# Kernel optimization log

Hardware: AMD Instinct MI355X
Metric: run time of the kernel (lower is better)

## Reference

```python
import jax, jax.numpy as jnp
import numpy as np
from jax import lax

P = 192      # patches per frame
PS = 7       # patch size
GH, GW = 16, 16  # grid cells
DS = 4       # encoder downsize factor
CH = 128     # feature channels
KS, PAD = 7, 3  # harris avg-pool kernel / padding


def _encoder(x, w, b):
    # stand-in encoder: conv(1->CH, k=7, stride=DS, pad=3) + relu
    y = lax.conv_general_dilated(x, w, (DS, DS), [(PAD, PAD), (PAD, PAD)],
                                 dimension_numbers=('NCHW', 'OIHW', 'NCHW'))
    return jax.nn.relu(y + b[None, :, None, None])


def _harris(frame):
    b, n, c, h, w = frame.shape
    f = frame.reshape(b * n, c, h, w)
    dx = jnp.pad(f[..., 1:] - f[..., :-1], ((0, 0), (0, 0), (0, 0), (0, 1)), mode='reflect')
    dy = jnp.pad(f[..., 1:, :] - f[..., :-1, :], ((0, 0), (0, 0), (0, 1), (0, 0)), mode='reflect')
    def avg(x):
        s = lax.reduce_window(x, 0.0, lax.add, (1, 1, KS, KS), (1, 1, 1, 1),
                              [(0, 0), (0, 0), (PAD, PAD), (PAD, PAD)])
        return s / (KS * KS)  # count_include_pad=True like torch avg_pool2d
    Ixx, Iyy, Ixy = avg(dx * dx), avg(dy * dy), avg(dx * dy)
    return (Ixx * Iyy - Ixy * Ixy) / (Ixx + Iyy + 1e-8)


def _best_coords(g):
    bn, _, h, w = g.shape
    ph = -(-h // GH); pw = -(-w // GW)
    g = jnp.pad(g, ((0, 0), (0, 0), (0, ph * GH - h), (0, pw * GW - w)))
    g = g.reshape(bn, GH, ph, GW, pw).transpose(0, 1, 3, 2, 4).reshape(bn, GH, GW, ph * pw)
    idx = jnp.argmax(g, axis=-1)
    vals = jnp.max(g, axis=-1)
    yg = idx // pw + (ph * jnp.arange(GH))[None, :, None]
    xg = idx % pw + (pw * jnp.arange(GW))[None, None, :]
    _, top = lax.top_k(vals.reshape(bn, -1), P)
    yb = jnp.take_along_axis(yg.reshape(bn, -1), top, 1)
    xb = jnp.take_along_axis(xg.reshape(bn, -1), top, 1)
    return jnp.stack([xb, yb], -1).astype(jnp.float32)  # (bn, P, 2)


def _bilinear(img, xs, ys):
    # img (c,h,w); xs,ys (N,) pixel coords; zero padding, align_corners=False
    c, h, w = img.shape
    x0 = jnp.floor(xs); y0 = jnp.floor(ys)
    wx = xs - x0; wy = ys - y0
    x0i = x0.astype(jnp.int32); y0i = y0.astype(jnp.int32)
    out = jnp.zeros((c, xs.shape[0]), img.dtype)
    for dxi, dyi, wt in ((0, 0, (1 - wx) * (1 - wy)), (1, 0, wx * (1 - wy)),
                         (0, 1, (1 - wx) * wy), (1, 1, wx * wy)):
        xi = x0i + dxi; yi = y0i + dyi
        m = ((xi >= 0) & (xi < w) & (yi >= 0) & (yi < h)).astype(img.dtype)
        v = img[:, jnp.clip(yi, 0, h - 1), jnp.clip(xi, 0, w - 1)]
        out = out + v * (wt * m)[None, :]
    return out


def _patches(coords, fmap, cmap):
    bn, c, h, w = fmap.shape
    coords = coords / DS
    r = jnp.arange(-(PS // 2), PS // 2 + 1, dtype=jnp.float32)
    dy, dx = jnp.meshgrid(r, r, indexing='ij')
    off = jnp.stack([dx, dy], -1)                       # (PS,PS,2)
    cp = coords[:, :, None, None, :] + off[None, None]  # (bn,P,PS,PS,2)
    xp = cp[..., 0].reshape(bn, -1); yp = cp[..., 1].reshape(bn, -1)
    pf = jax.vmap(_bilinear)(fmap, xp, yp)              # (bn,c,P*PS*PS)
    pf = pf.reshape(bn, c, P, PS * PS).transpose(0, 2, 1, 3)
    pc = jax.vmap(_bilinear)(cmap, coords[..., 0], coords[..., 1])  # (bn,c,P)
    pc = pc.transpose(0, 2, 1)
    return pf, pc


def setup_inputs() -> dict:
    key = jax.random.key(0)
    k1, k2, k3 = jax.random.split(key, 3)
    frame = jax.random.uniform(k1, (4, 2, 1, 480, 640), dtype=jnp.float32)
    w_f = jax.random.normal(k2, (CH, 1, KS, KS), dtype=jnp.float32) * 0.1
    w_c = jax.random.normal(k3, (CH, 1, KS, KS), dtype=jnp.float32) * 0.1
    b_f = jnp.zeros((CH,), jnp.float32)
    b_c = jnp.zeros((CH,), jnp.float32)
    return {"frame": frame, "w_f": w_f, "b_f": b_f, "w_c": w_c, "b_c": b_c}


def reference(frame, w_f, b_f, w_c, b_c):
    b, n, c, h, w = frame.shape
    f2 = frame.reshape(b * n, c, h, w)
    fmap = _encoder(f2, w_f, b_f)
    imap = _encoder(f2, w_c, b_c)
    g = _harris(frame)
    coords = _best_coords(g)
    patches_f, patches_c = _patches(coords, fmap, imap)
    return coords, patches_f, patches_c, fmap
```

## Files before the change

### kernel.cpp

```cpp
#include <hip/hip_runtime.h>
#include <hip/hip_bf16.h>
#include <math.h>

#define BN    8
#define H     480
#define W     640
#define CH    128
#define OH    120
#define OW    160
#define P     192
#define PS    7
#define GH    16
#define GW    16
#define PH    30
#define PW    40

__global__ __launch_bounds__(256) void conv_enc(
    const float* __restrict__ f,
    const float* __restrict__ wf, const float* __restrict__ bf,
    float* __restrict__ fmap)
{
    int pp = blockIdx.x * blockDim.x + threadIdx.x;
    if (pp >= BN * OH * (OW / 2)) return;
    int c0 = blockIdx.y * 16;
    int ox = 2 * (pp % (OW / 2));
    int t  = pp / (OW / 2);
    int oy = t % OH;
    int b  = t / OH;

    const float* fb = f + (size_t)b * H * W;
    int iy0 = 4 * oy - 3;
    int ix0 = 4 * ox - 3;

    float in[77];
    if (oy > 0 && ox > 0) {
        #pragma unroll
        for (int ky = 0; ky < 7; ky++) {
            const float* row = fb + (iy0 + ky) * W + ix0;
            #pragma unroll
            for (int kx = 0; kx < 11; kx++) in[ky * 11 + kx] = row[kx];
        }
    } else {
        #pragma unroll
        for (int ky = 0; ky < 7; ky++) {
            int iy = iy0 + ky;
            #pragma unroll
            for (int kx = 0; kx < 11; kx++) {
                int ix = ix0 + kx;
                in[ky * 11 + kx] = (iy >= 0 && ix >= 0) ? fb[iy * W + ix] : 0.0f;
            }
        }
    }

    const size_t plane = (size_t)(OH * OW);
    size_t obase = (size_t)b * CH * plane + (size_t)oy * OW + ox;
    #pragma unroll 1
    for (int c = c0; c < c0 + 16; c++) {
        const float* wfc = wf + c * 49;
        float bias = bf[c];
        float a0 = bias, a1 = bias;
        #pragma unroll
        for (int ky = 0; ky < 7; ky++) {
            #pragma unroll
            for (int kx = 0; kx < 7; kx++) {
                float wv = wfc[ky * 7 + kx];
                a0 = fmaf(wv, in[ky * 11 + kx],     a0);
                a1 = fmaf(wv, in[ky * 11 + kx + 4], a1);
            }
        }
        float2 r; r.x = fmaxf(a0, 0.0f); r.y = fmaxf(a1, 0.0f);
        *reinterpret_cast<float2*>(fmap + obase + (size_t)c * plane) = r;
    }
}

__global__ __launch_bounds__(256) void harris_cell(
    const float* __restrict__ f, float* __restrict__ cval, int* __restrict__ cidx)
{
    __shared__ float sf[37][48];
    __shared__ float dxx[36][48], dyy[36][48], dxy[36][48];
    __shared__ float sv[256];
    __shared__ int   si[256];

    int cell = blockIdx.x;
    int b  = cell >> 8;
    int ci = cell & 255;
    int gh = ci >> 4, gw = ci & 15;
    int cy0 = gh * PH, cx0 = gw * PW;
    const float* fb = f + (size_t)b * H * W;
    int tid = threadIdx.x;

    for (int i = tid; i < 37 * 47; i += 256) {
        int r = i / 47, c = i % 47;
        int y = min(max(cy0 - 3 + r, 0), H - 1);
        int x = min(max(cx0 - 3 + c, 0), W - 1);
        sf[r][c] = fb[(size_t)y * W + x];
    }
    __syncthreads();

    for (int i = tid; i < 36 * 46; i += 256) {
        int r = i / 46, c = i % 46;
        int y = cy0 - 3 + r;
        int x = cx0 - 3 + c;
        float vxx = 0.0f, vyy = 0.0f, vxy = 0.0f;
        if (y >= 0 && y < H && x >= 0 && x < W) {
            int xa = (x == W - 1) ? (x - 2) : x;
            int ya = (y == H - 1) ? (y - 2) : y;
            int lx = xa - (cx0 - 3);
            int ly = ya - (cy0 - 3);
            float dxv = sf[r][lx + 1] - sf[r][lx];
            float dyv = sf[ly + 1][c] - sf[ly][c];
            vxx = dxv * dxv;
            vyy = dyv * dyv;
            vxy = dxv * dyv;
        }
        dxx[r][c] = vxx; dyy[r][c] = vyy; dxy[r][c] = vxy;
    }
    __syncthreads();

    float best = -INFINITY;
    int   bidx = 0x7fffffff;
    if (tid < 200) {
        int col = tid % 40;
        int grp = tid / 40;
        int iy0 = grp * 6;
        float axx[6] = {0,0,0,0,0,0};
        float ayy[6] = {0,0,0,0,0,0};
        float axy[6] = {0,0,0,0,0,0};
        #pragma unroll
        for (int r = 0; r < 12; r++) {
            float vxx[7], vyy[7], vxy[7];
            #pragma unroll
            for (int kx = 0; kx < 7; kx++) {
                vxx[kx] = dxx[iy0 + r][col + kx];
                vyy[kx] = dyy[iy0 + r][col + kx];
                vxy[kx] = dxy[iy0 + r][col + kx];
            }
            #pragma unroll
            for (int p = 0; p < 6; p++) {
                if (r - p >= 0 && r - p <= 6) {
                    #pragma unroll
                    for (int kx = 0; kx < 7; kx++) {
                        axx[p] += vxx[kx];
                        ayy[p] += vyy[kx];
                        axy[p] += vxy[kx];
                    }
                }
            }
        }
        #pragma unroll
        for (int p = 0; p < 6; p++) {
            float Ixx = axx[p] / 49.0f;
            float Iyy = ayy[p] / 49.0f;
            float Ixy = axy[p] / 49.0f;
            float resp = (Ixx * Iyy - Ixy * Ixy) / (Ixx + Iyy + 1e-8f);
            int idx = (iy0 + p) * PW + col;
            if (resp > best) { best = resp; bidx = idx; }
        }
    }

    sv[tid] = best;
    si[tid] = bidx;
    __syncthreads();
    for (int s = 128; s > 0; s >>= 1) {
        if (tid < s) {
            float ov = sv[tid + s];
            int   oi = si[tid + s];
            if (ov > sv[tid] || (ov == sv[tid] && oi < si[tid])) {
                sv[tid] = ov; si[tid] = oi;
            }
        }
        __syncthreads();
    }
    if (tid == 0) { cval[cell] = sv[0]; cidx[cell] = si[0]; }
}

__global__ __launch_bounds__(256) void topk_coords(
    const float* __restrict__ cval, const int* __restrict__ cidx,
    float* __restrict__ coords)
{
    int b = blockIdx.x;
    int j = threadIdx.x;
    __shared__ float v[256];
    v[j] = cval[b * 256 + j];
    __syncthreads();
    float vj = v[j];
    int rank = 0;
    for (int k = 0; k < 256; k++) {
        float vk = v[k];
        rank += (vk > vj) || (vk == vj && k < j);
    }
    if (rank < P) {
        int ii = cidx[b * 256 + j];
        int gh = j >> 4, gw = j & 15;
        int y = ii / PW + gh * PH;
        int x = ii % PW + gw * PW;
        coords[((size_t)b * P + rank) * 2 + 0] = (float)x;
        coords[((size_t)b * P + rank) * 2 + 1] = (float)y;
    }
}

__global__ __launch_bounds__(256) void patches_kern(
    const float* __restrict__ coords,
    const float* __restrict__ fmap,
    const float* __restrict__ frame,
    const float* __restrict__ wc, const float* __restrict__ bc,
    float* __restrict__ pf, float* __restrict__ pc)
{
    __shared__ float sfm[CH][64];
    __shared__ float sf2[14][16];
    __shared__ float vq[CH][5];

    int bp = blockIdx.x;
    int b = bp / P;
    float cx = coords[(size_t)bp * 2 + 0] * 0.25f;
    float cy = coords[(size_t)bp * 2 + 1] * 0.25f;
    int tid = threadIdx.x;

    int X0 = (int)floorf(cx), Y0 = (int)floorf(cy);
    float wx = cx - (float)X0, wy = cy - (float)Y0;
    float w00 = (1.0f - wx) * (1.0f - wy);
    float w10 = wx * (1.0f - wy);
    float w01 = (1.0f - wx) * wy;
    float w11 = wx * wy;

    const float* fm = fmap + (size_t)b * CH * (OH * OW);
    for (int i = tid; i < CH * 64; i += 256) {
        int ch = i >> 6;
        int off = i & 63;
        int r = off >> 3, c = off & 7;
        int gy = Y0 - 3 + r, gx = X0 - 3 + c;
        sfm[ch][off] = (gy >= 0 && gy < OH && gx >= 0 && gx < OW)
                     ? fm[(size_t)ch * (OH * OW) + gy * OW + gx] : 0.0f;
    }

    int ix0 = 4 * X0 - 3, iy0 = 4 * Y0 - 3;
    const float* frb = frame + (size_t)b * H * W;
    for (int i = tid; i < 14 * 14; i += 256) {
        int r = i / 14, c = i % 14;
        int y = iy0 + r, x = ix0 + c;
        sf2[r][c] = (y >= 0 && y < H && x >= 0 && x < W)
                  ? frb[(size_t)y * W + x] : 0.0f;
    }
    __syncthreads();

    size_t pfbase = (size_t)bp * CH * 49;
    for (int idx = tid; idx < CH * 49; idx += 256) {
        int c = idx / 49;
        int k = idx - c * 49;
        int ky = k / 7, kx = k - ky * 7;
        int o = ky * 8 + kx;
        float acc = w00 * sfm[c][o]
                  + w10 * sfm[c][o + 1]
                  + w01 * sfm[c][o + 8]
                  + w11 * sfm[c][o + 9];
        pf[pfbase + idx] = acc;
    }

    for (int idx = tid; idx < 512; idx += 256) {
        int q = idx & 3;
        int c = idx >> 2;
        int qx = q & 1, qy = q >> 1;
        const float* wcc = wc + c * 49;
        float acc = bc[c];
        #pragma unroll
        for (int ky = 0; ky < 7; ky++) {
            #pragma unroll
            for (int kx = 0; kx < 7; kx++)
                acc = fmaf(wcc[ky * 7 + kx], sf2[4 * qy + ky][4 * qx + kx], acc);
        }
        vq[c][q] = fmaxf(acc, 0.0f);
    }
    __syncthreads();

    float m00 = (X0 >= 0 && X0 < OW && Y0 >= 0 && Y0 < OH) ? 1.0f : 0.0f;
    float m10 = (X0 + 1 >= 0 && X0 + 1 < OW && Y0 >= 0 && Y0 < OH) ? 1.0f : 0.0f;
    float m01 = (X0 >= 0 && X0 < OW && Y0 + 1 >= 0 && Y0 + 1 < OH) ? 1.0f : 0.0f;
    float m11 = (X0 + 1 >= 0 && X0 + 1 < OW && Y0 + 1 >= 0 && Y0 + 1 < OH) ? 1.0f : 0.0f;
    if (tid < CH) {
        float acc = w00 * m00 * vq[tid][0] + w10 * m10 * vq[tid][1]
                  + w01 * m01 * vq[tid][2] + w11 * m11 * vq[tid][3];
        pc[(size_t)bp * CH + tid] = acc;
    }
}

extern "C" void kernel_launch(void* const* d_in, const int* in_sizes, int n_in,
                              void* d_out, int out_size, void* d_ws, size_t ws_size,
                              hipStream_t stream)
{
    const float* frame = (const float*)d_in[0];
    const float* w_f   = (const float*)d_in[1];
    const float* b_f   = (const float*)d_in[2];
    const float* w_c   = (const float*)d_in[3];
    const float* b_c   = (const float*)d_in[4];

    float* out = (float*)d_out;
    const size_t coords_sz = (size_t)BN * P * 2;
    const size_t pf_sz     = (size_t)BN * P * CH * 49;
    const size_t pc_sz     = (size_t)BN * P * CH;
    float* coords = out;
    float* pf     = out + coords_sz;
    float* pc     = out + coords_sz + pf_sz;
    float* fmap   = out + coords_sz + pf_sz + pc_sz;

    float* cval = (float*)d_ws;
    int*   cidx = (int*)(cval + BN * 256);

    dim3 cg((BN * OH * (OW / 2)) / 256, 8);
    conv_enc<<<cg, 256, 0, stream>>>(frame, w_f, b_f, fmap);

    harris_cell<<<BN * 256, 256, 0, stream>>>(frame, cval, cidx);

    topk_coords<<<BN, 256, 0, stream>>>(cval, cidx, coords);

    patches_kern<<<BN * P, 256, 0, stream>>>(
        coords, fmap, frame, w_c, b_c, pf, pc);
}
```

Measured before the change: 252.6 us.

## Fuse encoder conv and Harris cell kernels into one interleaved launch

Merges the conv encoder and Harris cell-scoring kernels into one grid, interleaving conv and Harris blocks so the compute-heavy conv and the shared-memory Harris work can overlap on the GPU. This removes one kernel launch and the serialization between the two independent stages. In exchange, conv blocks now carry the Harris kernel's large static shared-memory allocation, which may reduce how many blocks fit on each compute unit.

New measurement: 315.2 us. +24.8%, slower.

```diff
diff --git a/kernel.cpp b/kernel.cpp
--- a/kernel.cpp
+++ b/kernel.cpp
@@ -15,79 +15,95 @@
 #define PH    30
 #define PW    40
 
-__global__ __launch_bounds__(256) void conv_enc(
+#define CONV_BLOCKS   2400
+#define HARRIS_BLOCKS 2048
+
+__global__ __launch_bounds__(256) void conv_harris(
     const float* __restrict__ f,
     const float* __restrict__ wf, const float* __restrict__ bf,
-    float* __restrict__ fmap)
-{
-    int pp = blockIdx.x * blockDim.x + threadIdx.x;
-    if (pp >= BN * OH * (OW / 2)) return;
-    int c0 = blockIdx.y * 16;
-    int ox = 2 * (pp % (OW / 2));
-    int t  = pp / (OW / 2);
-    int oy = t % OH;
-    int b  = t / OH;
-
-    const float* fb = f + (size_t)b * H * W;
-    int iy0 = 4 * oy - 3;
-    int ix0 = 4 * ox - 3;
-
-    float in[77];
-    if (oy > 0 && ox > 0) {
-        #pragma unroll
-        for (int ky = 0; ky < 7; ky++) {
-            const float* row = fb + (iy0 + ky) * W + ix0;
-            #pragma unroll
-            for (int kx = 0; kx < 11; kx++) in[ky * 11 + kx] = row[kx];
-        }
-    } else {
-        #pragma unroll
-        for (int ky = 0; ky < 7; ky++) {
-            int iy = iy0 + ky;
-            #pragma unroll
-            for (int kx = 0; kx < 11; kx++) {
-                int ix = ix0 + kx;
-                in[ky * 11 + kx] = (iy >= 0 && ix >= 0) ? fb[iy * W + ix] : 0.0f;
-            }
-        }
-    }
-
-    const size_t plane = (size_t)(OH * OW);
-    size_t obase = (size_t)b * CH * plane + (size_t)oy * OW + ox;
-    #pragma unroll 1
-    for (int c = c0; c < c0 + 16; c++) {
-        const float* wfc = wf + c * 49;
-        float bias = bf[c];
-        float a0 = bias, a1 = bias;
-        #pragma unroll
-        for (int ky = 0; ky < 7; ky++) {
-            #pragma unroll
-            for (int kx = 0; kx < 7; kx++) {
-                float wv = wfc[ky * 7 + kx];
-                a0 = fmaf(wv, in[ky * 11 + kx],     a0);
-                a1 = fmaf(wv, in[ky * 11 + kx + 4], a1);
-            }
-        }
-        float2 r; r.x = fmaxf(a0, 0.0f); r.y = fmaxf(a1, 0.0f);
-        *reinterpret_cast<float2*>(fmap + obase + (size_t)c * plane) = r;
-    }
-}
-
-__global__ __launch_bounds__(256) void harris_cell(
-    const float* __restrict__ f, float* __restrict__ cval, int* __restrict__ cidx)
+    float* __restrict__ fmap,
+    float* __restrict__ cval, int* __restrict__ cidx)
 {
     __shared__ float sf[37][48];
     __shared__ float dxx[36][48], dyy[36][48], dxy[36][48];
     __shared__ float sv[256];
     __shared__ int   si[256];
 
-    int cell = blockIdx.x;
+    int bid = blockIdx.x;
+    int tid = threadIdx.x;
+    bool is_conv;
+    int widx;
+    if (bid < 2 * HARRIS_BLOCKS) {
+        is_conv = (bid & 1) == 0;
+        widx = bid >> 1;
+    } else {
+        is_conv = true;
+        widx = HARRIS_BLOCKS + (bid - 2 * HARRIS_BLOCKS);
+    }
+
+    if (is_conv) {
+        int pb = widx % 300;
+        int cg = widx / 300;
+        int pp = pb * 256 + tid;
+        if (pp >= BN * OH * (OW / 2)) return;
+        int c0 = cg * 16;
+        int ox = 2 * (pp % (OW / 2));
+        int t  = pp / (OW / 2);
+        int oy = t % OH;
+        int b  = t / OH;
+
+        const float* fb = f + (size_t)b * H * W;
+        int iy0 = 4 * oy - 3;
+        int ix0 = 4 * ox - 3;
+
+        float in[77];
+        if (oy > 0 && ox > 0) {
+            #pragma unroll
+            for (int ky = 0; ky < 7; ky++) {
+                const float* row = fb + (iy0 + ky) * W + ix0;
+                #pragma unroll
+                for (int kx = 0; kx < 11; kx++) in[ky * 11 + kx] = row[kx];
+            }
+        } else {
+            #pragma unroll
+            for (int ky = 0; ky < 7; ky++) {
+                int iy = iy0 + ky;
+                #pragma unroll
+                for (int kx = 0; kx < 11; kx++) {
+                    int ix = ix0 + kx;
+                    in[ky * 11 + kx] = (iy >= 0 && ix >= 0) ? fb[iy * W + ix] : 0.0f;
+                }
+            }
+        }
+
+        const size_t plane = (size_t)(OH * OW);
+        size_t obase = (size_t)b * CH * plane + (size_t)oy * OW + ox;
+        #pragma unroll 1
+        for (int c = c0; c < c0 + 16; c++) {
+            const float* wfc = wf + c * 49;
+            float bias = bf[c];
+            float a0 = bias, a1 = bias;
+            #pragma unroll
+            for (int ky = 0; ky < 7; ky++) {
+                #pragma unroll
+                for (int kx = 0; kx < 7; kx++) {
+                    float wv = wfc[ky * 7 + kx];
+                    a0 = fmaf(wv, in[ky * 11 + kx],     a0);
+                    a1 = fmaf(wv, in[ky * 11 + kx + 4], a1);
+                }
+            }
+            float2 r; r.x = fmaxf(a0, 0.0f); r.y = fmaxf(a1, 0.0f);
+            *reinterpret_cast<float2*>(fmap + obase + (size_t)c * plane) = r;
+        }
+        return;
+    }
+
+    int cell = widx;
     int b  = cell >> 8;
     int ci = cell & 255;
     int gh = ci >> 4, gw = ci & 15;
     int cy0 = gh * PH, cx0 = gw * PW;
     const float* fb = f + (size_t)b * H * W;
-    int tid = threadIdx.x;
 
     for (int i = tid; i < 37 * 47; i += 256) {
         int r = i / 47, c = i % 47;
@@ -305,10 +321,8 @@
     float* cval = (float*)d_ws;
     int*   cidx = (int*)(cval + BN * 256);
 
-    dim3 cg((BN * OH * (OW / 2)) / 256, 8);
-    conv_enc<<<cg, 256, 0, stream>>>(frame, w_f, b_f, fmap);
-
-    harris_cell<<<BN * 256, 256, 0, stream>>>(frame, cval, cidx);
+    conv_harris<<<CONV_BLOCKS + HARRIS_BLOCKS, 256, 0, stream>>>(
+        frame, w_f, b_f, fmap, cval, cidx);
 
     topk_coords<<<BN, 256, 0, stream>>>(cval, cidx, coords);
 
```
